# Performance work log

Hardware: AMD Instinct MI355X
Metric: run time of the kernel (lower is better)

## Reference

```python
import jax, jax.numpy as jnp
import numpy as np

H, KVH, D, R = 32, 8, 128, 32
MASK_OUT = 0.5
NEG = -1e9  # stand-in for finfo.min to avoid -inf accumulation; preserves ordering/softmax
ROPE_THETA = 10000.0


def _rope_tables(S, D):
    inv = 1.0 / (ROPE_THETA ** (np.arange(0, D, 2, dtype=np.float32) / D))
    t = np.arange(S, dtype=np.float32)
    freqs = np.outer(t, inv)
    emb = np.concatenate([freqs, freqs], axis=-1)  # [S, D]
    return jnp.asarray(np.cos(emb)), jnp.asarray(np.sin(emb))


def _apply_rope(x, cos, sin):
    # x: [B,H,S,D]; cos/sin: [S,D]
    x1, x2 = jnp.split(x, 2, axis=-1)
    rot = jnp.concatenate([-x2, x1], axis=-1)
    return x * cos[None, None] + rot * sin[None, None]


def setup_inputs() -> dict:
    B, S, E = 1, 1024, 4096
    key = jax.random.key(0)
    ks = jax.random.split(key, 9)
    n = lambda k, shp, sc=0.02: jax.random.normal(k, shp, jnp.float32) * sc
    return {
        'hidden_states': n(ks[0], (B, S, E), 1.0),
        'wq': n(ks[1], (E, H * D)),
        'wk': n(ks[2], (E, KVH * D)),
        'wv': n(ks[3], (E, KVH * D)),
        'wo': n(ks[4], (H * D, E)),
        'mixq': n(ks[5], (E, R)),
        'mixk': n(ks[6], (E, R)),
        'q_pos': n(ks[7], (S, H, R, D)),
        'k_pos': n(ks[8], (S, H, R, D)),
    }


def reference(hidden_states, wq, wk, wv, wo, mixq, mixk, q_pos, k_pos):
    B, S, E = hidden_states.shape
    rep = H // KVH
    # QKV projections -> [B, heads, S, D]
    q = (hidden_states @ wq).reshape(B, S, H, D).transpose(0, 2, 1, 3)
    k = (hidden_states @ wk).reshape(B, S, KVH, D).transpose(0, 2, 1, 3)
    v = (hidden_states @ wv).reshape(B, S, KVH, D).transpose(0, 2, 1, 3)
    k = jnp.repeat(k, rep, axis=1)  # repeat_kv (GQA expand) -> [B,H,S,D]
    v = jnp.repeat(v, rep, axis=1)

    cos, sin = _rope_tables(S, D)
    qr = _apply_rope(q, cos, sin)
    kr = _apply_rope(k, cos, sin)
    scale = 1.0 / jnp.sqrt(jnp.float32(D))
    true_score = jnp.einsum('bhqd,bhkd->bhqk', qr, kr) * scale  # [B,H,S,S]

    # low-rank position-dependent draft score
    lrq = hidden_states @ mixq  # [B,S,R]
    lrk = hidden_states @ mixk
    pq = jnp.einsum('bmr,mhrd->bhmd', lrq, q_pos)  # [B,H,S,D]
    pk = jnp.einsum('bnr,nhrd->bhnd', lrk, k_pos)
    draft_score = jnp.einsum('bhqd,bhkd->bhqk', pq, pk)  # [B,H,S,S]

    causal = jnp.where(jnp.tril(jnp.ones((S, S), dtype=bool)), 0.0, NEG).astype(jnp.float32)[None, None]
    draft_score = draft_score + causal  # prefill: add causal mask to draft score

    num_remain = S - int(S * MASK_OUT)
    _, draft_idx = jax.lax.top_k(draft_score, num_remain)  # [B,H,S,K]

    # scatter 0 at kept kv positions, NEG elsewhere
    bi = jnp.arange(B)[:, None, None, None]
    hi = jnp.arange(H)[None, :, None, None]
    qi = jnp.arange(S)[None, None, :, None]
    topk_mask = jnp.full((B, H, S, S), NEG, jnp.float32).at[bi, hi, qi, draft_idx].set(0.0)

    probs = jax.nn.softmax(true_score + causal + topk_mask, axis=-1)
    out = jnp.einsum('bhqk,bhkd->bqhd', probs, v).reshape(B, S, H * D)
    return out @ wo
```

## Files before the change

kernel.cpp:

```cpp
#include <hip/hip_runtime.h>
#include <hip/hip_bf16.h>
#include <math.h>


typedef unsigned short u16;
using bf16x8 = __attribute__((ext_vector_type(8))) short;
using f32x4  = __attribute__((ext_vector_type(4))) float;

#define NEGBIG -1e30f

__device__ __forceinline__ unsigned int fkey(float f) {
    unsigned int u = __float_as_uint(f);
    return (u & 0x80000000u) ? ~u : (u | 0x80000000u);
}

__device__ __forceinline__ u16 f2b(float f) {
    union { float f; unsigned u; } x; x.f = f;
    unsigned r = x.u + 0x7fffu + ((x.u >> 16) & 1u);
    return (u16)(r >> 16);
}

__device__ __forceinline__ void gl_lds16(const u16* g, u16* l) {
    __builtin_amdgcn_global_load_lds(
        (__attribute__((address_space(1))) void*)(g),
        (__attribute__((address_space(3))) void*)(l), 16, 0, 0);
}

__global__ void rope_tables_kernel(float* __restrict__ cosb, float* __restrict__ sinb) {
    int t = blockIdx.x;
    int i = threadIdx.x;
    double inv = pow(10000.0, -((double)(2 * i)) / 128.0);
    double ang = (double)t * inv;
    cosb[t * 64 + i] = (float)cos(ang);
    sinb[t * 64 + i] = (float)sin(ang);
}

__global__ __launch_bounds__(256) void conv_bf16_kernel(const float* __restrict__ in, u16* __restrict__ out) {
    int i = blockIdx.x * 256 + threadIdx.x;
    float4 v = ((const float4*)in)[i];
    u16 o[4] = {f2b(v.x), f2b(v.y), f2b(v.z), f2b(v.w)};
    ((uint2*)out)[i] = *(const uint2*)o;
}

__device__ __forceinline__ void transpose_tile(
    const float* __restrict__ in, u16* __restrict__ out, int Kdim, int N,
    int bx, int by)
{
    __shared__ u16 tile[64][66];
    int n0 = bx * 64, k0 = by * 64;
    int t = threadIdx.x;
#pragma unroll
    for (int u = 0; u < 16; ++u) {
        int e = u * 256 + t; int r = e >> 6, c = e & 63;
        tile[r][c] = f2b(in[(size_t)(k0 + r) * N + n0 + c]);
    }
    __syncthreads();
#pragma unroll
    for (int u = 0; u < 16; ++u) {
        int e = u * 256 + t; int r = e >> 6, c = e & 63;
        out[(size_t)(n0 + r) * Kdim + k0 + c] = tile[c][r];
    }
}

__global__ __launch_bounds__(256) void transpose_bf16_kernel(
    const float* __restrict__ in, u16* __restrict__ out, int Kdim, int N)
{
    transpose_tile(in, out, Kdim, N, blockIdx.x, blockIdx.y);
}

__global__ __launch_bounds__(256) void transpose_qkvw_kernel(
    const float* __restrict__ wq, const float* __restrict__ wk, const float* __restrict__ wv,
    u16* __restrict__ wqT, u16* __restrict__ wkT, u16* __restrict__ wvT)
{
    int bx = blockIdx.x;
    const float* in; u16* outp; int N;
    if (bx < 64)      { in = wq; outp = wqT; N = 4096; }
    else if (bx < 80) { in = wk; outp = wkT; N = 1024; bx -= 64; }
    else              { in = wv; outp = wvT; N = 1024; bx -= 80; }
    transpose_tile(in, outp, 4096, N, bx, blockIdx.y);
}

__global__ __launch_bounds__(128) void rope_pack2_kernel(
    const float* __restrict__ qb, const float* __restrict__ kb,
    const float* __restrict__ cosb, const float* __restrict__ sinb,
    u16* __restrict__ qr, u16* __restrict__ kr)
{
    int s = blockIdx.x, h = blockIdx.y, d = threadIdx.x;
    const float* src; u16* dst; int W; float scale;
    if (h < 32) { src = qb; dst = qr; W = 4096; scale = 0.08838834764831845f; }
    else        { h -= 32; src = kb; dst = kr; W = 1024; scale = 1.0f; }
    float x  = src[(size_t)s * W + h * 128 + d];
    float x2 = src[(size_t)s * W + h * 128 + (d ^ 64)];
    float cs = cosb[s * 64 + (d & 63)];
    float sn = sinb[s * 64 + (d & 63)];
    float rot = (d < 64) ? -x2 : x2;
    dst[((size_t)h * 1024 + s) * 128 + d] = f2b((x * cs + rot * sn) * scale);
}

__device__ __forceinline__ void gemm_bf16_tile(
    const u16* __restrict__ A, const u16* __restrict__ BT, float* __restrict__ C,
    int Kdim, int Ncols, int bm, int bn)
{
    __shared__ u16 As[128 * 32];
    __shared__ u16 Bs[128 * 32];
    const int t = threadIdx.x;
    const int wave = t >> 6, lane = t & 63;
    const int wr = wave >> 1, wc = wave & 1;
    const int fr = lane & 15, fq = lane >> 4;

    f32x4 acc[4][4];
#pragma unroll
    for (int m = 0; m < 4; ++m)
#pragma unroll
        for (int n = 0; n < 4; ++n) acc[m][n] = 0.f;

    const int srow = 32 * wave + (lane >> 2);
    const int skc = (lane & 3) * 8;
    const u16* aS = A  + ((size_t)(bm * 128) + srow) * Kdim + skc;
    const u16* bS = BT + ((size_t)(bn * 128) + srow) * Kdim + skc;
    u16* aD0 = As + 1024 * wave;  u16* aD1 = aD0 + 512;
    u16* bD0 = Bs + 1024 * wave;  u16* bD1 = bD0 + 512;

    const int aoff = (wr * 64 + fr) * 32 + fq * 8;
    const int boff = (wc * 64 + fr) * 32 + fq * 8;

    for (int k0 = 0; k0 < Kdim; k0 += 32) {
        __syncthreads();
        gl_lds16(aS + k0, aD0);
        gl_lds16(aS + (size_t)16 * Kdim + k0, aD1);
        gl_lds16(bS + k0, bD0);
        gl_lds16(bS + (size_t)16 * Kdim + k0, bD1);
        __syncthreads();

        bf16x8 af[4], bfr[4];
#pragma unroll
        for (int m = 0; m < 4; ++m) af[m] = *(const bf16x8*)(As + aoff + m * 512);
#pragma unroll
        for (int n = 0; n < 4; ++n) bfr[n] = *(const bf16x8*)(Bs + boff + n * 512);
#pragma unroll
        for (int m = 0; m < 4; ++m)
#pragma unroll
            for (int n = 0; n < 4; ++n)
                acc[m][n] = __builtin_amdgcn_mfma_f32_16x16x32_bf16(af[m], bfr[n], acc[m][n], 0, 0, 0);
    }

    float* Cb = C + (size_t)(bm * 128 + wr * 64 + fq * 4) * Ncols + bn * 128 + wc * 64 + fr;
#pragma unroll
    for (int m = 0; m < 4; ++m)
#pragma unroll
        for (int j = 0; j < 4; ++j)
#pragma unroll
            for (int n = 0; n < 4; ++n)
                Cb[(size_t)(m * 16 + j) * Ncols + n * 16] = acc[m][n][j];
}

__global__ __launch_bounds__(256) void gemm_qkv_bf16_kernel(
    const u16* __restrict__ hs_bf, const u16* __restrict__ wqT,
    const u16* __restrict__ wkT, const u16* __restrict__ wvT,
    float* __restrict__ q, float* __restrict__ k, float* __restrict__ v)
{
    int bn = blockIdx.x, bm = blockIdx.y;
    const u16* Bsel; float* Csel; int Ncols;
    if (bn < 32)      { Bsel = wqT; Csel = q; Ncols = 4096; }
    else if (bn < 40) { Bsel = wkT; Csel = k; Ncols = 1024; bn -= 32; }
    else              { Bsel = wvT; Csel = v; Ncols = 1024; bn -= 40; }
    gemm_bf16_tile(hs_bf, Bsel, Csel, 4096, Ncols, bm, bn);
}

__global__ __launch_bounds__(256) void gemm_wo_bf16_kernel(
    const u16* __restrict__ attn_bf, const u16* __restrict__ woT, float* __restrict__ out)
{
    gemm_bf16_tile(attn_bf, woT, out, 4096, 4096, blockIdx.y, blockIdx.x);
}

__global__ __launch_bounds__(256) void lr_kernel(
    const float* __restrict__ hs, const float* __restrict__ mixq, const float* __restrict__ mixk,
    float* __restrict__ lrq, float* __restrict__ lrk)
{
    __shared__ float row[4096];
    __shared__ float part[2][32][4];
    int m = blockIdx.x, t = threadIdx.x;
#pragma unroll
    for (int u = 0; u < 4; ++u)
        ((float4*)row)[t + u * 256] = ((const float4*)(hs + (size_t)m * 4096))[t + u * 256];
    __syncthreads();
    int r = t & 31, which = (t >> 5) & 1, quarter = t >> 6;
    const float* mix = which ? mixk : mixq;
    float acc = 0.f;
    int kbase = quarter * 1024;
#pragma unroll 8
    for (int kk = 0; kk < 1024; ++kk)
        acc = fmaf(row[kbase + kk], mix[(size_t)(kbase + kk) * 32 + r], acc);
    part[which][r][quarter] = acc;
    __syncthreads();
    if (t < 64) {
        int r2 = t & 31, w2 = t >> 5;
        float s = part[w2][r2][0] + part[w2][r2][1] + part[w2][r2][2] + part[w2][r2][3];
        (w2 ? lrk : lrq)[(size_t)m * 32 + r2] = s;
    }
}

__global__ __launch_bounds__(128) void ppos_kernel(
    const float* __restrict__ lr, const float* __restrict__ pos,
    float* __restrict__ out, int mbase)
{
    int h = blockIdx.x, m = blockIdx.y + mbase, d = threadIdx.x;
    __shared__ float lrs[32];
    if (d < 32) lrs[d] = lr[(size_t)m * 32 + d];
    __syncthreads();
    const float* base = pos + ((size_t)(m * 32 + h) * 32) * 128 + d;
    float acc = 0.f;
#pragma unroll
    for (int r = 0; r < 32; ++r)
        acc = fmaf(lrs[r], base[(size_t)r * 128], acc);
    out[((size_t)h * 1024 + m) * 128 + d] = acc;
}

__global__ __launch_bounds__(256) void draft_gemm_kernel(
    const float* __restrict__ pq, const float* __restrict__ pk,
    float* __restrict__ scores, int h0)
{
    int idx = blockIdx.x;
    int bm, bn;
    if (idx < 5)       { bm = 4; bn = idx; }
    else if (idx < 11) { bm = 5; bn = idx - 5; }
    else if (idx < 18) { bm = 6; bn = idx - 11; }
    else               { bm = 7; bn = idx - 18; }
    int hh = blockIdx.y;

    const float* A  = pq + ((size_t)(h0 + hh) * 1024 + bm * 128) * 128;
    const float* BT = pk + ((size_t)(h0 + hh) * 1024 + bn * 128) * 128;
    float* C = scores + ((size_t)hh * 512 + (bm - 4) * 128) * 1024 + bn * 128;

    __shared__ float As[8][128];
    __shared__ float Bs[8][128];
    const int t = threadIdx.x;
    const int tx = t & 15, ty = (t >> 4) & 15;

    float acc[8][8];
#pragma unroll
    for (int u = 0; u < 8; ++u)
#pragma unroll
        for (int w = 0; w < 8; ++w) acc[u][w] = 0.f;

    const int ai = t >> 1;
    const int ah = (t & 1) * 4;
    const float* Ap = A + (size_t)ai * 128 + ah;
    const float* Bp = BT + (size_t)ai * 128 + ah;

    for (int k0 = 0; k0 < 128; k0 += 8) {
        float4 av = *(const float4*)(Ap + k0);
        float4 bv = *(const float4*)(Bp + k0);
        __syncthreads();
        As[ah + 0][ai] = av.x; As[ah + 1][ai] = av.y;
        As[ah + 2][ai] = av.z; As[ah + 3][ai] = av.w;
        Bs[ah + 0][ai] = bv.x; Bs[ah + 1][ai] = bv.y;
        Bs[ah + 2][ai] = bv.z; Bs[ah + 3][ai] = bv.w;
        __syncthreads();
#pragma unroll
        for (int kk = 0; kk < 8; ++kk) {
            float4 a0 = *(const float4*)(&As[kk][ty * 4]);
            float4 a1 = *(const float4*)(&As[kk][64 + ty * 4]);
            float4 b0 = *(const float4*)(&Bs[kk][tx * 4]);
            float4 b1 = *(const float4*)(&Bs[kk][64 + tx * 4]);
            float aa[8] = {a0.x, a0.y, a0.z, a0.w, a1.x, a1.y, a1.z, a1.w};
            float bb[8] = {b0.x, b0.y, b0.z, b0.w, b1.x, b1.y, b1.z, b1.w};
#pragma unroll
            for (int u = 0; u < 8; ++u)
#pragma unroll
                for (int w = 0; w < 8; ++w)
                    acc[u][w] = fmaf(aa[u], bb[w], acc[u][w]);
        }
    }
#pragma unroll
    for (int u = 0; u < 8; ++u) {
        int row = (u < 4) ? (ty * 4 + u) : (64 + ty * 4 + (u - 4));
        *(float4*)(C + (size_t)row * 1024 + tx * 4)
            = make_float4(acc[u][0], acc[u][1], acc[u][2], acc[u][3]);
        *(float4*)(C + (size_t)row * 1024 + 64 + tx * 4)
            = make_float4(acc[u][4], acc[u][5], acc[u][6], acc[u][7]);
    }
}

__global__ __launch_bounds__(256) void topk_select_kernel(
    const float* __restrict__ scores, int h0,
    unsigned long long* __restrict__ mask)
{
    int qt = blockIdx.x, hh = blockIdx.y;
    int h = h0 + hh;
    int t = threadIdx.x;
    const int i = t >> 4, jj = t & 15;
    const int lrow = qt * 16 + i;
    const int qrow = 512 + lrow;

    const float* src = scores + ((size_t)hh * 512 + lrow) * 1024;

    unsigned int vals[64];
#pragma unroll
    for (int n = 0; n < 64; ++n) {
        int col = 16 * n + jj;
        float s = src[col];
        vals[n] = fkey(col <= qrow ? s : NEGBIG);
    }

    unsigned int p = 0u;
    int kth = 512;
    for (int b = 31; b >= 0; --b) {
        unsigned int bit = 1u << b;
        unsigned int himask = (b == 31) ? 0u : (0xFFFFFFFFu << (b + 1));
        int cnt = 0;
#pragma unroll
        for (int n = 0; n < 64; ++n)
            cnt += (int)((((vals[n] ^ p) & himask) == 0u) && ((vals[n] & bit) != 0u));
        cnt += __shfl_xor(cnt, 1);
        cnt += __shfl_xor(cnt, 2);
        cnt += __shfl_xor(cnt, 4);
        cnt += __shfl_xor(cnt, 8);
        if (cnt >= kth) p |= bit; else kth -= cnt;
    }

    unsigned long long wpart[16];
#pragma unroll
    for (int w = 0; w < 16; ++w) wpart[w] = 0ull;
#pragma unroll
    for (int n = 0; n < 64; ++n) {
        int w = n >> 2;
        int bpos = ((n & 3) << 4) + jj;
        wpart[w] |= ((unsigned long long)(vals[n] >= p)) << bpos;
    }
#pragma unroll
    for (int s = 1; s < 16; s <<= 1) {
#pragma unroll
        for (int w = 0; w < 16; ++w)
            wpart[w] |= __shfl_xor(wpart[w], s);
    }
    mask[((size_t)h * 1024 + qrow) * 16 + jj] = wpart[jj];
}

#define ATTN_KP 136
#define ATTN_VP 72

__global__ __launch_bounds__(256) void attn_mfma_kernel(
    const u16* __restrict__ qr,
    const u16* __restrict__ kr,
    const u16* __restrict__ vT,
    const unsigned long long* __restrict__ mask,
    u16* __restrict__ attn)
{
    int bx = blockIdx.x;
    int qt = (bx & 1) ? (bx >> 1) : (15 - (bx >> 1));
    int h = blockIdx.y;
    int kvh = h >> 2;
    int q0 = qt * 64;
    int t = threadIdx.x;
    int wave = t >> 6, lane = t & 63;
    int fr = lane & 15, fq = lane >> 4;
    int qrow = q0 + wave * 16 + fr;

    __shared__ u16 Ks[64 * ATTN_KP];
    __shared__ u16 Vs[128 * ATTN_VP];

    bf16x8 qf[4];
    const u16* qbase = qr + ((size_t)h * 1024 + qrow) * 128 + fq * 8;
#pragma unroll
    for (int kc = 0; kc < 4; ++kc)
        qf[kc] = *(const bf16x8*)(qbase + kc * 32);

    float m_run = -3.0e38f, l_run = 0.f;
    f32x4 accO[8];
#pragma unroll
    for (int m2 = 0; m2 < 8; ++m2) accO[m2] = 0.f;

    const unsigned long long* mrow = mask + ((size_t)h * 1024 + qrow) * 16;
    const bool use_mask = (qrow >= 512);
    const u16* kgh = kr + (size_t)kvh * 1024 * 128;
    const u16* vgh = vT + (size_t)kvh * 128 * 1024;

    int ntiles = qt + 1;
    for (int c = 0; c < ntiles; ++c) {
        int kv0 = c * 64;
        __syncthreads();
#pragma unroll
        for (int u = 0; u < 4; ++u) {
            int e = t + u * 256;
            int row = e >> 4, bc = (e & 15) * 8;
            uint4 d4 = *(const uint4*)(kgh + ((size_t)(kv0 + row)) * 128 + bc);
            *(uint4*)(&Ks[row * ATTN_KP + bc]) = d4;
        }
#pragma unroll
        for (int u = 0; u < 4; ++u) {
            int e = t + u * 256;
            int row = e >> 3, bc = (e & 7) * 8;
            uint4 d4 = *(const uint4*)(vgh + (size_t)row * 1024 + kv0 + bc);
            *(uint4*)(&Vs[row * ATTN_VP + bc]) = d4;
        }
        __syncthreads();

        f32x4 accS[4];
        accS[0] = 0.f; accS[1] = 0.f; accS[2] = 0.f; accS[3] = 0.f;
#pragma unroll
        for (int t2 = 0; t2 < 4; ++t2)
#pragma unroll
            for (int kc = 0; kc < 4; ++kc) {
                bf16x8 kf = *(const bf16x8*)(&Ks[(t2 * 16 + fr) * ATTN_KP + kc * 32 + fq * 8]);
                accS[t2] = __builtin_amdgcn_mfma_f32_16x16x32_bf16(kf, qf[kc], accS[t2], 0, 0, 0);
            }

        unsigned long long mw = use_mask ? mrow[c] : ~0ull;
        float p[4][4];
        float tmax = -3.0e38f;
#pragma unroll
        for (int t2 = 0; t2 < 4; ++t2)
#pragma unroll
            for (int j = 0; j < 4; ++j) {
                int kvi = (t2 << 4) + (fq << 2) + j;
                bool ok = ((mw >> kvi) & 1ull) && (kv0 + kvi <= qrow);
                float s = ok ? accS[t2][j] : -3.0e38f;
                p[t2][j] = s;
                tmax = fmaxf(tmax, s);
            }
        tmax = fmaxf(tmax, __shfl_xor(tmax, 16));
        tmax = fmaxf(tmax, __shfl_xor(tmax, 32));
        float m_new = fmaxf(m_run, tmax);
        float sf = __expf(m_run - m_new);
        float psum = 0.f;
#pragma unroll
        for (int t2 = 0; t2 < 4; ++t2)
#pragma unroll
            for (int j = 0; j < 4; ++j) {
                float e = (p[t2][j] > -1.0e38f) ? __expf(p[t2][j] - m_new) : 0.f;
                p[t2][j] = e;
                psum += e;
            }
        psum += __shfl_xor(psum, 16);
        psum += __shfl_xor(psum, 32);
        l_run = l_run * sf + psum;
        m_run = m_new;

#pragma unroll
        for (int m2 = 0; m2 < 8; ++m2) accO[m2] *= sf;

        union { uint4 u; bf16x8 b; } pc[2];
        int srcA = fr + ((fq & 1) << 5);
        int srcB = srcA + 16;
        bool hi = (fq & 2) != 0;
#pragma unroll
        for (int half = 0; half < 2; ++half) {
            unsigned W0, W1, W2, W3;
            asm("v_cvt_pk_bf16_f32 %0, %1, %2" : "=v"(W0) : "v"(p[2 * half][0]),     "v"(p[2 * half][1]));
            asm("v_cvt_pk_bf16_f32 %0, %1, %2" : "=v"(W1) : "v"(p[2 * half][2]),     "v"(p[2 * half][3]));
            asm("v_cvt_pk_bf16_f32 %0, %1, %2" : "=v"(W2) : "v"(p[2 * half + 1][0]), "v"(p[2 * half + 1][1]));
            asm("v_cvt_pk_bf16_f32 %0, %1, %2" : "=v"(W3) : "v"(p[2 * half + 1][2]), "v"(p[2 * half + 1][3]));
            unsigned a0 = __shfl(W0, srcA), a1 = __shfl(W1, srcA);
            unsigned a2 = __shfl(W2, srcA), a3 = __shfl(W3, srcA);
            unsigned b0 = __shfl(W0, srcB), b1 = __shfl(W1, srcB);
            unsigned b2 = __shfl(W2, srcB), b3 = __shfl(W3, srcB);
            pc[half].u.x = hi ? a2 : a0;
            pc[half].u.y = hi ? a3 : a1;
            pc[half].u.z = hi ? b2 : b0;
            pc[half].u.w = hi ? b3 : b1;
        }

#pragma unroll
        for (int m2 = 0; m2 < 8; ++m2) {
            bf16x8 vf0 = *(const bf16x8*)(&Vs[(m2 * 16 + fr) * ATTN_VP + fq * 8]);
            accO[m2] = __builtin_amdgcn_mfma_f32_16x16x32_bf16(vf0, pc[0].b, accO[m2], 0, 0, 0);
            bf16x8 vf1 = *(const bf16x8*)(&Vs[(m2 * 16 + fr) * ATTN_VP + 32 + fq * 8]);
            accO[m2] = __builtin_amdgcn_mfma_f32_16x16x32_bf16(vf1, pc[1].b, accO[m2], 0, 0, 0);
        }
    }

    float il = 1.0f / l_run;
    u16* obase = attn + (size_t)qrow * 4096 + h * 128 + fq * 4;
#pragma unroll
    for (int m2 = 0; m2 < 8; ++m2) {
        uint2 st;
        st.x = (unsigned)f2b(accO[m2][0] * il) | ((unsigned)f2b(accO[m2][1] * il) << 16);
        st.y = (unsigned)f2b(accO[m2][2] * il) | ((unsigned)f2b(accO[m2][3] * il) << 16);
        *(uint2*)(obase + m2 * 16) = st;
    }
}

extern "C" void kernel_launch(void* const* d_in, const int* in_sizes, int n_in,
                              void* d_out, int out_size, void* d_ws, size_t ws_size,
                              hipStream_t stream)
{
    (void)in_sizes; (void)n_in; (void)out_size; (void)ws_size;
    const float* hs   = (const float*)d_in[0];
    const float* wq   = (const float*)d_in[1];
    const float* wk   = (const float*)d_in[2];
    const float* wv   = (const float*)d_in[3];
    const float* wo   = (const float*)d_in[4];
    const float* mixq = (const float*)d_in[5];
    const float* mixk = (const float*)d_in[6];
    const float* qpos = (const float*)d_in[7];
    const float* kpos = (const float*)d_in[8];
    float* out = (float*)d_out;

    float* ws   = (float*)d_ws;
    float* qb   = ws;
    float* kb   = qb + 4194304;
    float* vb   = kb + 1048576;
    float* pq   = vb + 1048576;
    float* pk   = pq + 4194304;
    float* lrq  = pk + 4194304;
    float* lrk  = lrq + 32768;
    float* cosb = lrk + 32768;
    float* sinb = cosb + 65536;
    unsigned long long* mask = (unsigned long long*)(sinb + 65536);
    u16* hs_bf = (u16*)(ws + 14876672 + 1048576);
    u16* wkT   = hs_bf + 4194304;
    u16* wvT   = wkT + 4194304;
    u16* wqT   = (u16*)pq;
    u16* woT   = (u16*)pq;
    u16* qr_bf = (u16*)pq;
    u16* kr_bf = (u16*)pk;
    u16* vT_bf = (u16*)(pk + 1048576);
    u16* attn_bf = hs_bf;
    float* scores = (float*)hs_bf;

    hipLaunchKernelGGL(rope_tables_kernel, dim3(1024), dim3(64), 0, stream, cosb, sinb);
    hipLaunchKernelGGL(conv_bf16_kernel, dim3(4096), dim3(256), 0, stream, hs, hs_bf);
    hipLaunchKernelGGL(transpose_qkvw_kernel, dim3(96, 64), dim3(256), 0, stream,
                       wq, wk, wv, wqT, wkT, wvT);
    hipLaunchKernelGGL(gemm_qkv_bf16_kernel, dim3(48, 8), dim3(256), 0, stream,
                       hs_bf, wqT, wkT, wvT, qb, kb, vb);
    hipLaunchKernelGGL(lr_kernel, dim3(1024), dim3(256), 0, stream, hs, mixq, mixk, lrq, lrk);
    hipLaunchKernelGGL(ppos_kernel, dim3(32, 512), dim3(128), 0, stream, lrq, qpos, pq, 512);
    hipLaunchKernelGGL(ppos_kernel, dim3(32, 1024), dim3(128), 0, stream, lrk, kpos, pk, 0);
    for (int h0 = 0; h0 < 32; h0 += 8) {
        hipLaunchKernelGGL(draft_gemm_kernel, dim3(26, 8), dim3(256), 0, stream,
                           pq, pk, scores, h0);
        hipLaunchKernelGGL(topk_select_kernel, dim3(32, 8), dim3(256), 0, stream,
                           scores, h0, mask);
    }
    hipLaunchKernelGGL(rope_pack2_kernel, dim3(1024, 40), dim3(128), 0, stream,
                       qb, kb, cosb, sinb, qr_bf, kr_bf);
    hipLaunchKernelGGL(transpose_bf16_kernel, dim3(16, 16), dim3(256), 0, stream, vb, vT_bf, 1024, 1024);
    hipLaunchKernelGGL(attn_mfma_kernel, dim3(16, 32), dim3(256), 0, stream,
                       qr_bf, kr_bf, vT_bf, mask, attn_bf);
    hipLaunchKernelGGL(transpose_bf16_kernel, dim3(64, 64), dim3(256), 0, stream, wo, woT, 4096, 4096);
    hipLaunchKernelGGL(gemm_wo_bf16_kernel, dim3(32, 8), dim3(256), 0, stream,
                       attn_bf, woT, out);
}
```

Before: 805.2 us.

## Merge init and ppos launches, halve draft GEMM tile width, vectorize topk loads

```diff
diff --git a/kernel.cpp b/kernel.cpp
--- a/kernel.cpp
+++ b/kernel.cpp
@@ -26,20 +26,24 @@
         (__attribute__((address_space(3))) void*)(l), 16, 0, 0);
 }
 
-__global__ void rope_tables_kernel(float* __restrict__ cosb, float* __restrict__ sinb) {
-    int t = blockIdx.x;
-    int i = threadIdx.x;
-    double inv = pow(10000.0, -((double)(2 * i)) / 128.0);
-    double ang = (double)t * inv;
-    cosb[t * 64 + i] = (float)cos(ang);
-    sinb[t * 64 + i] = (float)sin(ang);
-}
-
-__global__ __launch_bounds__(256) void conv_bf16_kernel(const float* __restrict__ in, u16* __restrict__ out) {
-    int i = blockIdx.x * 256 + threadIdx.x;
-    float4 v = ((const float4*)in)[i];
-    u16 o[4] = {f2b(v.x), f2b(v.y), f2b(v.z), f2b(v.w)};
-    ((uint2*)out)[i] = *(const uint2*)o;
+__global__ __launch_bounds__(256) void init_kernel(
+    const float* __restrict__ hs, u16* __restrict__ hs_bf,
+    float* __restrict__ cosb, float* __restrict__ sinb)
+{
+    int bx = blockIdx.x, t = threadIdx.x;
+    if (bx < 4096) {
+        int i = bx * 256 + t;
+        float4 v = ((const float4*)hs)[i];
+        u16 o[4] = {f2b(v.x), f2b(v.y), f2b(v.z), f2b(v.w)};
+        ((uint2*)hs_bf)[i] = *(const uint2*)o;
+    } else {
+        int row = (bx - 4096) * 4 + (t >> 6);
+        int i = t & 63;
+        double inv = pow(10000.0, -((double)(2 * i)) / 128.0);
+        double ang = (double)row * inv;
+        cosb[row * 64 + i] = (float)cos(ang);
+        sinb[row * 64 + i] = (float)sin(ang);
+    }
 }
 
 __device__ __forceinline__ void transpose_tile(
@@ -200,11 +204,15 @@
     }
 }
 
-__global__ __launch_bounds__(128) void ppos_kernel(
-    const float* __restrict__ lr, const float* __restrict__ pos,
-    float* __restrict__ out, int mbase)
-{
-    int h = blockIdx.x, m = blockIdx.y + mbase, d = threadIdx.x;
+__global__ __launch_bounds__(128) void ppos2_kernel(
+    const float* __restrict__ lrq, const float* __restrict__ lrk,
+    const float* __restrict__ qpos, const float* __restrict__ kpos,
+    float* __restrict__ pq, float* __restrict__ pk)
+{
+    int h = blockIdx.x, by = blockIdx.y, d = threadIdx.x;
+    const float* lr; const float* pos; float* outp; int m;
+    if (by < 512) { m = 512 + by; lr = lrq; pos = qpos; outp = pq; }
+    else          { m = by - 512; lr = lrk; pos = kpos; outp = pk; }
     __shared__ float lrs[32];
     if (d < 32) lrs[d] = lr[(size_t)m * 32 + d];
     __syncthreads();
@@ -213,7 +221,7 @@
 #pragma unroll
     for (int r = 0; r < 32; ++r)
         acc = fmaf(lrs[r], base[(size_t)r * 128], acc);
-    out[((size_t)h * 1024 + m) * 128 + d] = acc;
+    outp[((size_t)h * 1024 + m) * 128 + d] = acc;
 }
 
 __global__ __launch_bounds__(256) void draft_gemm_kernel(
@@ -221,55 +229,54 @@
     float* __restrict__ scores, int h0)
 {
     int idx = blockIdx.x;
-    int bm, bn;
-    if (idx < 5)       { bm = 4; bn = idx; }
-    else if (idx < 11) { bm = 5; bn = idx - 5; }
-    else if (idx < 18) { bm = 6; bn = idx - 11; }
-    else               { bm = 7; bn = idx - 18; }
+    int bm, bc;
+    if (idx < 10)      { bm = 4; bc = idx; }
+    else if (idx < 22) { bm = 5; bc = idx - 10; }
+    else if (idx < 36) { bm = 6; bc = idx - 22; }
+    else               { bm = 7; bc = idx - 36; }
     int hh = blockIdx.y;
 
     const float* A  = pq + ((size_t)(h0 + hh) * 1024 + bm * 128) * 128;
-    const float* BT = pk + ((size_t)(h0 + hh) * 1024 + bn * 128) * 128;
-    float* C = scores + ((size_t)hh * 512 + (bm - 4) * 128) * 1024 + bn * 128;
+    const float* BT = pk + ((size_t)(h0 + hh) * 1024 + bc * 64) * 128;
+    float* C = scores + ((size_t)hh * 512 + (bm - 4) * 128) * 1024 + bc * 64;
 
     __shared__ float As[8][128];
-    __shared__ float Bs[8][128];
+    __shared__ float Bs[8][64];
     const int t = threadIdx.x;
     const int tx = t & 15, ty = (t >> 4) & 15;
 
-    float acc[8][8];
+    float acc[8][4];
 #pragma unroll
     for (int u = 0; u < 8; ++u)
 #pragma unroll
-        for (int w = 0; w < 8; ++w) acc[u][w] = 0.f;
-
-    const int ai = t >> 1;
-    const int ah = (t & 1) * 4;
+        for (int w = 0; w < 4; ++w) acc[u][w] = 0.f;
+
+    const int ai = t >> 1, ah = (t & 1) * 4;
+    const int bi = t >> 2, bh = (t & 3) * 2;
     const float* Ap = A + (size_t)ai * 128 + ah;
-    const float* Bp = BT + (size_t)ai * 128 + ah;
+    const float* Bp = BT + (size_t)bi * 128 + bh;
 
     for (int k0 = 0; k0 < 128; k0 += 8) {
         float4 av = *(const float4*)(Ap + k0);
-        float4 bv = *(const float4*)(Bp + k0);
+        float2 bv = *(const float2*)(Bp + k0);
         __syncthreads();
         As[ah + 0][ai] = av.x; As[ah + 1][ai] = av.y;
         As[ah + 2][ai] = av.z; As[ah + 3][ai] = av.w;
-        Bs[ah + 0][ai] = bv.x; Bs[ah + 1][ai] = bv.y;
-        Bs[ah + 2][ai] = bv.z; Bs[ah + 3][ai] = bv.w;
+        Bs[bh][bi] = bv.x; Bs[bh + 1][bi] = bv.y;
         __syncthreads();
 #pragma unroll
         for (int kk = 0; kk < 8; ++kk) {
             float4 a0 = *(const float4*)(&As[kk][ty * 4]);
             float4 a1 = *(const float4*)(&As[kk][64 + ty * 4]);
             float4 b0 = *(const float4*)(&Bs[kk][tx * 4]);
-            float4 b1 = *(const float4*)(&Bs[kk][64 + tx * 4]);
             float aa[8] = {a0.x, a0.y, a0.z, a0.w, a1.x, a1.y, a1.z, a1.w};
-            float bb[8] = {b0.x, b0.y, b0.z, b0.w, b1.x, b1.y, b1.z, b1.w};
-#pragma unroll
-            for (int u = 0; u < 8; ++u)
-#pragma unroll
-                for (int w = 0; w < 8; ++w)
-                    acc[u][w] = fmaf(aa[u], bb[w], acc[u][w]);
+#pragma unroll
+            for (int u = 0; u < 8; ++u) {
+                acc[u][0] = fmaf(aa[u], b0.x, acc[u][0]);
+                acc[u][1] = fmaf(aa[u], b0.y, acc[u][1]);
+                acc[u][2] = fmaf(aa[u], b0.z, acc[u][2]);
+                acc[u][3] = fmaf(aa[u], b0.w, acc[u][3]);
+            }
         }
     }
 #pragma unroll
@@ -277,8 +284,6 @@
         int row = (u < 4) ? (ty * 4 + u) : (64 + ty * 4 + (u - 4));
         *(float4*)(C + (size_t)row * 1024 + tx * 4)
             = make_float4(acc[u][0], acc[u][1], acc[u][2], acc[u][3]);
-        *(float4*)(C + (size_t)row * 1024 + 64 + tx * 4)
-            = make_float4(acc[u][4], acc[u][5], acc[u][6], acc[u][7]);
     }
 }
 
@@ -297,10 +302,13 @@
 
     unsigned int vals[64];
 #pragma unroll
-    for (int n = 0; n < 64; ++n) {
-        int col = 16 * n + jj;
-        float s = src[col];
-        vals[n] = fkey(col <= qrow ? s : NEGBIG);
+    for (int g = 0; g < 16; ++g) {
+        float4 v = *(const float4*)(src + g * 64 + jj * 4);
+        int col = g * 64 + jj * 4;
+        vals[g * 4 + 0] = fkey((col + 0) <= qrow ? v.x : NEGBIG);
+        vals[g * 4 + 1] = fkey((col + 1) <= qrow ? v.y : NEGBIG);
+        vals[g * 4 + 2] = fkey((col + 2) <= qrow ? v.z : NEGBIG);
+        vals[g * 4 + 3] = fkey((col + 3) <= qrow ? v.w : NEGBIG);
     }
 
     unsigned int p = 0u;
@@ -323,11 +331,10 @@
 #pragma unroll
     for (int w = 0; w < 16; ++w) wpart[w] = 0ull;
 #pragma unroll
-    for (int n = 0; n < 64; ++n) {
-        int w = n >> 2;
-        int bpos = ((n & 3) << 4) + jj;
-        wpart[w] |= ((unsigned long long)(vals[n] >= p)) << bpos;
-    }
+    for (int g = 0; g < 16; ++g)
+#pragma unroll
+        for (int e = 0; e < 4; ++e)
+            wpart[g] |= ((unsigned long long)(vals[g * 4 + e] >= p)) << (4 * jj + e);
 #pragma unroll
     for (int s = 1; s < 16; s <<= 1) {
 #pragma unroll
@@ -341,8 +348,7 @@
 #define ATTN_VP 72
 
 __global__ __launch_bounds__(256) void attn_mfma_kernel(
-    const u16* __restrict__ qr,
-    const u16* __restrict__ kr,
+    const u16* __restrict__ qr, const u16* __restrict__ kr,
     const u16* __restrict__ vT,
     const unsigned long long* __restrict__ mask,
     u16* __restrict__ attn)
@@ -383,16 +389,16 @@
 #pragma unroll
         for (int u = 0; u < 4; ++u) {
             int e = t + u * 256;
-            int row = e >> 4, bc = (e & 15) * 8;
-            uint4 d4 = *(const uint4*)(kgh + ((size_t)(kv0 + row)) * 128 + bc);
-            *(uint4*)(&Ks[row * ATTN_KP + bc]) = d4;
+            int row = e >> 4, bc2 = (e & 15) * 8;
+            uint4 d4 = *(const uint4*)(kgh + ((size_t)(kv0 + row)) * 128 + bc2);
+            *(uint4*)(&Ks[row * ATTN_KP + bc2]) = d4;
         }
 #pragma unroll
         for (int u = 0; u < 4; ++u) {
             int e = t + u * 256;
-            int row = e >> 3, bc = (e & 7) * 8;
-            uint4 d4 = *(const uint4*)(vgh + (size_t)row * 1024 + kv0 + bc);
-            *(uint4*)(&Vs[row * ATTN_VP + bc]) = d4;
+            int row = e >> 3, bc2 = (e & 7) * 8;
+            uint4 d4 = *(const uint4*)(vgh + (size_t)row * 1024 + kv0 + bc2);
+            *(uint4*)(&Vs[row * ATTN_VP + bc2]) = d4;
         }
         __syncthreads();
 
@@ -519,17 +525,16 @@
     u16* attn_bf = hs_bf;
     float* scores = (float*)hs_bf;
 
-    hipLaunchKernelGGL(rope_tables_kernel, dim3(1024), dim3(64), 0, stream, cosb, sinb);
-    hipLaunchKernelGGL(conv_bf16_kernel, dim3(4096), dim3(256), 0, stream, hs, hs_bf);
+    hipLaunchKernelGGL(init_kernel, dim3(4352), dim3(256), 0, stream, hs, hs_bf, cosb, sinb);
     hipLaunchKernelGGL(transpose_qkvw_kernel, dim3(96, 64), dim3(256), 0, stream,
                        wq, wk, wv, wqT, wkT, wvT);
     hipLaunchKernelGGL(gemm_qkv_bf16_kernel, dim3(48, 8), dim3(256), 0, stream,
                        hs_bf, wqT, wkT, wvT, qb, kb, vb);
     hipLaunchKernelGGL(lr_kernel, dim3(1024), dim3(256), 0, stream, hs, mixq, mixk, lrq, lrk);
-    hipLaunchKernelGGL(ppos_kernel, dim3(32, 512), dim3(128), 0, stream, lrq, qpos, pq, 512);
-    hipLaunchKernelGGL(ppos_kernel, dim3(32, 1024), dim3(128), 0, stream, lrk, kpos, pk, 0);
+    hipLaunchKernelGGL(ppos2_kernel, dim3(32, 1536), dim3(128), 0, stream,
+                       lrq, lrk, qpos, kpos, pq, pk);
     for (int h0 = 0; h0 < 32; h0 += 8) {
-        hipLaunchKernelGGL(draft_gemm_kernel, dim3(26, 8), dim3(256), 0, stream,
+        hipLaunchKernelGGL(draft_gemm_kernel, dim3(52, 8), dim3(256), 0, stream,
                            pq, pk, scores, h0);
         hipLaunchKernelGGL(topk_select_kernel, dim3(32, 8), dim3(256), 0, stream,
                            scores, h0, mask);
```

Result: faster. 748.5 us (-7.0%).
